# Performance work log

Measured on AMD Instinct MI355X. Metric: run time of the kernel, lower is better.

The kernel has to match this reference:

```python
import jax, jax.numpy as jnp
import numpy as np

B, T, D, H = 2, 2048, 2048, 16
HS = D // H  # head size 128


def setup_inputs() -> dict:
    key = jax.random.key(0)
    ks = jax.random.split(key, 5)
    s = 0.02
    return {
        "x": jax.random.normal(ks[0], (B, T, D), dtype=jnp.float32),
        "wq": jax.random.normal(ks[1], (D, D), dtype=jnp.float32) * s,
        "wk": jax.random.normal(ks[2], (D, D), dtype=jnp.float32) * s,
        "wv": jax.random.normal(ks[3], (D, D), dtype=jnp.float32) * s,
        "wo": jax.random.normal(ks[4], (D, D), dtype=jnp.float32) * s,
    }


def reference(x, wq, wk, wv, wo):
    b, t, d = x.shape
    # projections: nn.Linear(x) = x @ W.T ; here W stored as (out,in)
    q = (x @ wq.T).reshape(b, t, H, HS).transpose(0, 2, 1, 3)  # (B,H,T,HS)
    k = (x @ wk.T).reshape(b, t, H, HS).transpose(0, 2, 1, 3)
    v = (x @ wv.T).reshape(b, t, H, HS).transpose(0, 2, 1, 3)
    scale = 1.0 / np.sqrt(HS).astype(np.float32)
    e = jnp.einsum("bhqd,bhkd->bhqk", q, k) * scale  # (B,H,T,T)
    causal = jnp.tril(jnp.ones((t, t), dtype=bool))
    e = jnp.where(causal[None, None], e, jnp.float32(-jnp.inf))
    alpha = jax.nn.softmax(e, axis=-1)  # dropout=0.0 -> identity
    attn = jnp.einsum("bhqk,bhkd->bhqd", alpha, v)
    attn = attn.transpose(0, 2, 1, 3).reshape(b, t, d)
    return attn @ wo.T
```

## Files before the change

kernel.cpp:

```cpp
#include <hip/hip_runtime.h>
#include <hip/hip_bf16.h>

typedef __bf16 bf16x8 __attribute__((ext_vector_type(8)));
typedef float f32x4 __attribute__((ext_vector_type(4)));
typedef unsigned short u16x8 __attribute__((ext_vector_type(8)));

#define GLDS16(g, s)                                                         \
  __builtin_amdgcn_global_load_lds(                                          \
      (const __attribute__((address_space(1))) void*)(g),                    \
      (__attribute__((address_space(3))) void*)(s), 16, 0, 0)

__device__ __forceinline__ void store1(__hip_bfloat16* p, float v) { *p = __float2bfloat16(v); }
__device__ __forceinline__ void store1(float* p, float v) { *p = v; }

__global__ __launch_bounds__(256) void cast_f32_to_bf16(const float4* __restrict__ in,
                                                        ushort4* __restrict__ out, int n4) {
  int i = blockIdx.x * 256 + threadIdx.x;
  if (i >= n4) return;
  float4 v = in[i];
  union { ushort4 u; __hip_bfloat16 h[4]; } o;
  o.h[0] = __float2bfloat16(v.x);
  o.h[1] = __float2bfloat16(v.y);
  o.h[2] = __float2bfloat16(v.z);
  o.h[3] = __float2bfloat16(v.w);
  out[i] = o.u;
}

__global__ __launch_bounds__(256) void cast4_f32_to_bf16(const float4* __restrict__ w0,
                                                         const float4* __restrict__ w1,
                                                         const float4* __restrict__ w2,
                                                         const float4* __restrict__ w3,
                                                         ushort4* __restrict__ o0,
                                                         ushort4* __restrict__ o1,
                                                         ushort4* __restrict__ o2,
                                                         ushort4* __restrict__ o3, int n4) {
  int i = blockIdx.x * 256 + threadIdx.x;
  if (i >= n4) return;
  int s = blockIdx.y;
  const float4* in = (s == 0) ? w0 : (s == 1) ? w1 : (s == 2) ? w2 : w3;
  ushort4* out = (s == 0) ? o0 : (s == 1) ? o1 : (s == 2) ? o2 : o3;
  float4 v = in[i];
  union { ushort4 u; __hip_bfloat16 h[4]; } o;
  o.h[0] = __float2bfloat16(v.x);
  o.h[1] = __float2bfloat16(v.y);
  o.h[2] = __float2bfloat16(v.z);
  o.h[3] = __float2bfloat16(v.w);
  out[i] = o.u;
}

template <typename OutT>
__global__ __launch_bounds__(512, 2) void gemm256(const __hip_bfloat16* __restrict__ A,
                                                  const __hip_bfloat16* __restrict__ B0,
                                                  const __hip_bfloat16* __restrict__ B1,
                                                  const __hip_bfloat16* __restrict__ B2,
                                                  OutT* __restrict__ C0,
                                                  OutT* __restrict__ C1,
                                                  OutT* __restrict__ C2,
                                                  int nBx, int nBy, int ntPerMat,
                                                  int N, int K) {
  __shared__ __hip_bfloat16 As[2][256 * 64];
  __shared__ __hip_bfloat16 Bs[2][256 * 64];

  const int t = threadIdx.x;
  const int w = t >> 6, l = t & 63;
  const int lr = l & 15, hi = l >> 4;

  const int nwg = nBx * nBy;
  int id = (int)blockIdx.x;
  id = (id & 7) * (nwg >> 3) + (id >> 3);
  const int bx = id / nBy;
  const int by = id % nBy;

  const int sel = bx / ntPerMat;
  const __hip_bfloat16* Bm = (sel == 0) ? B0 : ((sel == 1) ? B1 : B2);
  OutT* Cm = (sel == 0) ? C0 : ((sel == 1) ? C1 : C2);
  const int n0 = (bx - sel * ntPerMat) * 256;
  const int m0 = by * 256;

  const int c0r = t >> 3, cs = t & 7;
  const int c1r = 64 + c0r;
  const __hip_bfloat16* aP0 = A + (size_t)(m0 + c0r) * K + (cs ^ (c0r & 7)) * 8;
  const __hip_bfloat16* aP1 = A + (size_t)(m0 + c1r) * K + (cs ^ (c1r & 7)) * 8;
  const __hip_bfloat16* bP0 = Bm + (size_t)(n0 + c0r) * K + (cs ^ (c0r & 7)) * 8;
  const __hip_bfloat16* bP1 = Bm + (size_t)(n0 + c1r) * K + (cs ^ (c1r & 7)) * 8;
  const size_t HK = (size_t)128 * K;

#define STAGE_S(sidx, nb, koff)                                              \
  do {                                                                       \
    if ((sidx) == 0) {                                                       \
      GLDS16(aP0 + (koff), (char*)As[nb] + t * 16);                          \
      GLDS16(aP1 + (koff), (char*)As[nb] + 8192 + t * 16);                   \
    } else if ((sidx) == 1) {                                                \
      GLDS16(bP0 + (koff), (char*)Bs[nb] + t * 16);                          \
      GLDS16(bP1 + (koff), (char*)Bs[nb] + 8192 + t * 16);                   \
    } else if ((sidx) == 2) {                                                \
      GLDS16(aP0 + HK + (koff), (char*)As[nb] + 16384 + t * 16);             \
      GLDS16(aP1 + HK + (koff), (char*)As[nb] + 24576 + t * 16);             \
    } else {                                                                 \
      GLDS16(bP0 + HK + (koff), (char*)Bs[nb] + 16384 + t * 16);             \
      GLDS16(bP1 + HK + (koff), (char*)Bs[nb] + 24576 + t * 16);             \
    }                                                                        \
  } while (0)

  f32x4 acc[2][2][4][2] = {};
  bf16x8 afA[4][2], afB[4][2];
  bf16x8 bqA[2][2], bqB[2][2];
  const int NT = K / 64;
  const int sw = lr & 7;
  const int arow = (w >> 2) * 64;
  const int brow = (w & 3) * 32;

#define RD_A(dst, mh)                                                        \
  _Pragma("unroll") for (int mi = 0; mi < 4; ++mi)                           \
    _Pragma("unroll") for (int kk = 0; kk < 2; ++kk)                         \
      dst[mi][kk] = *(const bf16x8*)((const char*)As[buf] +                  \
          ((mh) * 128 + arow + mi * 16 + lr) * 128 + (((kk * 4 + hi) ^ sw) << 4));
#define RD_B(dst, nh)                                                        \
  _Pragma("unroll") for (int ni = 0; ni < 2; ++ni)                           \
    _Pragma("unroll") for (int kk = 0; kk < 2; ++kk)                         \
      dst[ni][kk] = *(const bf16x8*)((const char*)Bs[buf] +                  \
          ((nh) * 128 + brow + ni * 16 + lr) * 128 + (((kk * 4 + hi) ^ sw) << 4));
#define MFMA_Q(mh, nh, afv, bq)                                              \
  do {                                                                       \
    __builtin_amdgcn_s_setprio(1);                                           \
    _Pragma("unroll") for (int mi = 0; mi < 4; ++mi)                         \
      _Pragma("unroll") for (int ni = 0; ni < 2; ++ni) {                     \
        acc[mh][nh][mi][ni] = __builtin_amdgcn_mfma_f32_16x16x32_bf16(       \
            afv[mi][0], bq[ni][0], acc[mh][nh][mi][ni], 0, 0, 0);            \
        acc[mh][nh][mi][ni] = __builtin_amdgcn_mfma_f32_16x16x32_bf16(       \
            afv[mi][1], bq[ni][1], acc[mh][nh][mi][ni], 0, 0, 0);            \
      }                                                                      \
    __builtin_amdgcn_s_setprio(0);                                           \
  } while (0)
#define WAITV(n)  asm volatile("s_waitcnt vmcnt(" #n ")" ::: "memory")

  STAGE_S(0, 0, 0);
  STAGE_S(1, 0, 0);
  STAGE_S(3, 0, 0);
  STAGE_S(2, 0, 0);

  for (int tt = 0; tt < NT; ++tt) {
    const int buf = tt & 1, nb = buf ^ 1;
    const bool stg = (tt + 1 < NT);
    const size_t ko = (size_t)(tt + 1) * 64;

    WAITV(2);
    __builtin_amdgcn_s_barrier();
    RD_A(afA, 0);
    RD_B(bqA, 0);
    RD_B(bqB, 1);
    if (stg) { STAGE_S(0, nb, ko); STAGE_S(1, nb, ko); }
    MFMA_Q(0, 0, afA, bqA);
    MFMA_Q(0, 1, afA, bqB);

    if (stg) WAITV(4); else WAITV(0);
    __builtin_amdgcn_s_barrier();
    RD_A(afB, 1);
    if (stg) { STAGE_S(3, nb, ko); STAGE_S(2, nb, ko); }
    MFMA_Q(1, 1, afB, bqB);
    MFMA_Q(1, 0, afB, bqA);
  }
#undef WAITV
#undef MFMA_Q
#undef RD_B
#undef RD_A
#undef STAGE_S

#pragma unroll
  for (int mh = 0; mh < 2; ++mh)
#pragma unroll
    for (int nh = 0; nh < 2; ++nh)
#pragma unroll
      for (int mi = 0; mi < 4; ++mi)
#pragma unroll
        for (int ni = 0; ni < 2; ++ni)
#pragma unroll
          for (int i = 0; i < 4; ++i) {
            size_t idx = (size_t)(m0 + mh * 128 + arow + mi * 16 + hi * 4 + i) * N +
                         (n0 + nh * 128 + brow + ni * 16 + lr);
            store1(&Cm[idx], acc[mh][nh][mi][ni][i]);
          }
}

__global__ __launch_bounds__(256, 2) void flash_attn(const __hip_bfloat16* __restrict__ Qg,
                                                     const __hip_bfloat16* __restrict__ Kg,
                                                     const __hip_bfloat16* __restrict__ Vg,
                                                     __hip_bfloat16* __restrict__ Og) {
  __shared__ __hip_bfloat16 Ks[2][64 * 128];
  __shared__ __hip_bfloat16 Vt[128 * 64];

  const int mblk = blockIdx.x;
  const int bh = mblk & 31;
  const int jj = mblk >> 5;
  const int qt = (jj < 8) ? (15 - jj) : (jj - 8);
  const int b = bh >> 4, h = bh & 15;
  const int q0 = qt * 128;
  const int t = threadIdx.x, w = t >> 6, l = t & 63;
  const int lr = l & 15, hi = l >> 4;
  const size_t base = ((size_t)b * 2048) * 2048 + (size_t)h * 128;
  const int nt = 2 * qt + 2;
  const float scale = 0.08838834764831843f;

  const int hi2 = (hi & 1) * 2;
  const int addrA = (((hi2) << 4) | lr) << 2;
  const int addrB = (((hi2 + 1) << 4) | lr) << 2;
  int addr_o[4];
#pragma unroll
  for (int i = 0; i < 4; ++i) addr_o[i] = ((l & 48) | (hi * 4 + i)) << 2;
  const bool hiHigh = (hi >> 1) != 0;

  bf16x8 qf[2][4];
#pragma unroll
  for (int g = 0; g < 2; ++g) {
    const __hip_bfloat16* qrow = Qg + base + (size_t)(q0 + w * 32 + g * 16 + lr) * 2048;
#pragma unroll
    for (int kk = 0; kk < 4; ++kk)
      qf[g][kk] = *(const bf16x8*)(qrow + kk * 32 + hi * 8);
  }

  f32x4 o_acc[2][8] = {};
  float m_run[2] = {-1e30f, -1e30f};
  float l_run[2] = {0.f, 0.f};

  const __hip_bfloat16* kptr[4];
#pragma unroll
  for (int i = 0; i < 4; ++i) {
    int c = i * 256 + t;
    int kr = c >> 4;
    int ke = ((c & 15) ^ (kr & 7)) * 8;
    kptr[i] = Kg + base + (size_t)kr * 2048 + ke;
  }
  const __hip_bfloat16* vptr[2];
#pragma unroll
  for (int it = 0; it < 2; ++it) {
    int kp = it * 16 + w * 4 + hi;
    vptr[it] = Vg + base + (size_t)(kp * 2) * 2048 + lr * 8;
  }

  u16x8 va[2], vb[2];
#pragma unroll
  for (int i = 0; i < 4; ++i)
    GLDS16(kptr[i], (char*)Ks[0] + (i * 256 + t) * 16);
#pragma unroll
  for (int it = 0; it < 2; ++it) {
    va[it] = *(const u16x8*)vptr[it];
    vb[it] = *(const u16x8*)(vptr[it] + 2048);
  }

  for (int kt = 0; kt < nt; ++kt) {
    const int cur = kt & 1;
    const int kb = kt * 64;
    __syncthreads();

#pragma unroll
    for (int it = 0; it < 2; ++it)
#pragma unroll
      for (int j2 = 0; j2 < 8; ++j2) {
        int d = lr * 8 + j2;
        int sw = (lr ^ j2) & 7;
        int off = d * 128 + (((it * 4 + w) ^ sw) << 4) + hi * 4;
        *(unsigned int*)((char*)Vt + off) =
            (unsigned int)va[it][j2] | ((unsigned int)vb[it][j2] << 16);
      }
    if (kt + 1 < nt) {
      const size_t adv = (size_t)(kb + 64) * 2048;
#pragma unroll
      for (int i = 0; i < 4; ++i)
        GLDS16(kptr[i] + adv, (char*)Ks[cur ^ 1] + (i * 256 + t) * 16);
#pragma unroll
      for (int it = 0; it < 2; ++it) {
        va[it] = *(const u16x8*)(vptr[it] + adv);
        vb[it] = *(const u16x8*)(vptr[it] + adv + 2048);
      }
    }
    asm volatile("s_waitcnt lgkmcnt(0)" ::: "memory");
    __builtin_amdgcn_s_barrier();

    if (!(kt == nt - 1 && w < 2)) {
      const char* ks = (const char*)Ks[cur];

      f32x4 st[2][4];
#pragma unroll
      for (int g = 0; g < 2; ++g)
#pragma unroll
        for (int nk = 0; nk < 4; ++nk) { f32x4 z = {}; st[g][nk] = z; }
#pragma unroll
      for (int nk = 0; nk < 4; ++nk)
#pragma unroll
        for (int kk = 0; kk < 4; ++kk) {
          bf16x8 kf = *(const bf16x8*)(ks + (nk * 16 + lr) * 256 +
                                       (((kk * 4 + hi) ^ (lr & 7)) << 4));
#pragma unroll
          for (int g = 0; g < 2; ++g)
            st[g][nk] = __builtin_amdgcn_mfma_f32_16x16x32_bf16(kf, qf[g][kk], st[g][nk], 0, 0, 0);
        }

      const bool maskt = (kt >= nt - 2);
#pragma unroll
      for (int g = 0; g < 2; ++g)
#pragma unroll
        for (int nk = 0; nk < 4; ++nk)
#pragma unroll
          for (int i = 0; i < 4; ++i) {
            float v = st[g][nk][i] * scale;
            if (maskt) {
              int ki = kb + nk * 16 + hi * 4 + i;
              int qi = q0 + w * 32 + g * 16 + lr;
              if (ki > qi) v = -1e30f;
            }
            st[g][nk][i] = v;
          }

      bf16x8 paf[2][2];
#pragma unroll
      for (int g = 0; g < 2; ++g) {
        float t0 = fmaxf(fmaxf(st[g][0][0], st[g][0][1]), fmaxf(st[g][0][2], st[g][0][3]));
        float t1 = fmaxf(fmaxf(st[g][1][0], st[g][1][1]), fmaxf(st[g][1][2], st[g][1][3]));
        float t2 = fmaxf(fmaxf(st[g][2][0], st[g][2][1]), fmaxf(st[g][2][2], st[g][2][3]));
        float t3 = fmaxf(fmaxf(st[g][3][0], st[g][3][1]), fmaxf(st[g][3][2], st[g][3][3]));
        float mx = fmaxf(fmaxf(t0, t1), fmaxf(t2, t3));
        mx = fmaxf(mx, __shfl_xor(mx, 16));
        mx = fmaxf(mx, __shfl_xor(mx, 32));

        if (!__all(mx - m_run[g] <= 8.0f)) {
          float mnew = fmaxf(m_run[g], mx);
          float rs = __expf(m_run[g] - mnew);
          m_run[g] = mnew;
          l_run[g] *= rs;
          int rsi = __float_as_int(rs);
#pragma unroll
          for (int i = 0; i < 4; ++i) {
            float rso = __int_as_float(__builtin_amdgcn_ds_bpermute(addr_o[i], rsi));
#pragma unroll
            for (int nc = 0; nc < 8; ++nc) o_acc[g][nc][i] *= rso;
          }
        }

#pragma unroll
        for (int nk = 0; nk < 4; ++nk)
#pragma unroll
          for (int i = 0; i < 4; ++i)
            st[g][nk][i] = __expf(st[g][nk][i] - m_run[g]);

        float s0 = (st[g][0][0] + st[g][0][1]) + (st[g][0][2] + st[g][0][3]);
        float s1 = (st[g][1][0] + st[g][1][1]) + (st[g][1][2] + st[g][1][3]);
        float s2 = (st[g][2][0] + st[g][2][1]) + (st[g][2][2] + st[g][2][3]);
        float s3 = (st[g][3][0] + st[g][3][1]) + (st[g][3][2] + st[g][3][3]);
        float sm = (s0 + s1) + (s2 + s3);
        sm += __shfl_xor(sm, 16);
        sm += __shfl_xor(sm, 32);
        l_run[g] += sm;

        unsigned pk[4][2];
#pragma unroll
        for (int nk = 0; nk < 4; ++nk) {
          asm("v_cvt_pk_bf16_f32 %0, %1, %2"
              : "=v"(pk[nk][0]) : "v"(st[g][nk][0]), "v"(st[g][nk][1]));
          asm("v_cvt_pk_bf16_f32 %0, %1, %2"
              : "=v"(pk[nk][1]) : "v"(st[g][nk][2]), "v"(st[g][nk][3]));
        }

#pragma unroll
        for (int kk = 0; kk < 2; ++kk) {
          unsigned au[4];
#pragma unroll
          for (int p = 0; p < 4; ++p) {
            int ad = (p < 2) ? addrA : addrB;
            int v0 = __builtin_amdgcn_ds_bpermute(ad, (int)pk[2 * kk][p & 1]);
            int v1 = __builtin_amdgcn_ds_bpermute(ad, (int)pk[2 * kk + 1][p & 1]);
            au[p] = hiHigh ? (unsigned)v1 : (unsigned)v0;
          }
          union { unsigned u[4]; bf16x8 v; } cv;
          cv.u[0] = au[0]; cv.u[1] = au[1]; cv.u[2] = au[2]; cv.u[3] = au[3];
          paf[g][kk] = cv.v;
        }
      }

#pragma unroll
      for (int kk = 0; kk < 2; ++kk)
#pragma unroll
        for (int nc = 0; nc < 8; ++nc) {
          int d = nc * 16 + lr;
          int sw = ((d >> 3) ^ d) & 7;
          bf16x8 vfr = *(const bf16x8*)((const char*)Vt + d * 128 +
                                        (((kk * 4 + hi) ^ sw) << 4));
#pragma unroll
          for (int g = 0; g < 2; ++g)
            o_acc[g][nc] = __builtin_amdgcn_mfma_f32_16x16x32_bf16(paf[g][kk], vfr, o_acc[g][nc], 0, 0, 0);
        }
    }
  }

#pragma unroll
  for (int g = 0; g < 2; ++g) {
    float lo[4];
#pragma unroll
    for (int i = 0; i < 4; ++i)
      lo[i] = __int_as_float(__builtin_amdgcn_ds_bpermute(addr_o[i], __float_as_int(l_run[g])));
#pragma unroll
    for (int nc = 0; nc < 8; ++nc)
#pragma unroll
      for (int i = 0; i < 4; ++i) {
        float val = o_acc[g][nc][i] / lo[i];
        Og[base + (size_t)(q0 + w * 32 + g * 16 + hi * 4 + i) * 2048 + nc * 16 + lr] =
            __float2bfloat16(val);
      }
  }
}

extern "C" void kernel_launch(void* const* d_in, const int* in_sizes, int n_in,
                              void* d_out, int out_size, void* d_ws, size_t ws_size,
                              hipStream_t stream) {
  const float* x  = (const float*)d_in[0];
  const float* wq = (const float*)d_in[1];
  const float* wk = (const float*)d_in[2];
  const float* wv = (const float*)d_in[3];
  const float* wo = (const float*)d_in[4];
  float* out = (float*)d_out;

  const int BT = 4096, D = 2048;
  const size_t ND = (size_t)D * D;
  const size_t NX = (size_t)BT * D;

  __hip_bfloat16* xb  = (__hip_bfloat16*)d_ws;
  __hip_bfloat16* wqb = xb + NX;
  __hip_bfloat16* wkb = wqb + ND;
  __hip_bfloat16* wvb = wkb + ND;
  __hip_bfloat16* wob = wvb + ND;
  __hip_bfloat16* Qb  = wob + ND;
  __hip_bfloat16* Kb  = Qb + NX;
  __hip_bfloat16* Vb  = Kb + NX;
  __hip_bfloat16* Ab  = Vb + NX;

  cast_f32_to_bf16<<<(int)(NX / 4 / 256), 256, 0, stream>>>((const float4*)x, (ushort4*)xb, (int)(NX / 4));
  cast4_f32_to_bf16<<<dim3((int)(ND / 4 / 256), 4), 256, 0, stream>>>(
      (const float4*)wq, (const float4*)wk, (const float4*)wv, (const float4*)wo,
      (ushort4*)wqb, (ushort4*)wkb, (ushort4*)wvb, (ushort4*)wob, (int)(ND / 4));

  gemm256<__hip_bfloat16><<<384, 512, 0, stream>>>(
      xb, wqb, wkb, wvb, Qb, Kb, Vb, 24, 16, 8, D, D);

  flash_attn<<<512, 256, 0, stream>>>(Qb, Kb, Vb, Ab);

  gemm256<float><<<128, 512, 0, stream>>>(
      Ab, wob, wob, wob, out, out, out, 8, 16, 8, D, D);
}
```

Before: 282.1 us.

## Issue all next-tile loads upfront and prefetch LDS fragments into registers

After: 282.8 us. No clear change (+0.2%).

```diff
diff --git a/kernel.cpp b/kernel.cpp
--- a/kernel.cpp
+++ b/kernel.cpp
@@ -110,15 +110,15 @@
   const int arow = (w >> 2) * 64;
   const int brow = (w & 3) * 32;
 
-#define RD_A(dst, mh)                                                        \
+#define RD_A(dst, mh, bb)                                                    \
   _Pragma("unroll") for (int mi = 0; mi < 4; ++mi)                           \
     _Pragma("unroll") for (int kk = 0; kk < 2; ++kk)                         \
-      dst[mi][kk] = *(const bf16x8*)((const char*)As[buf] +                  \
+      dst[mi][kk] = *(const bf16x8*)((const char*)As[bb] +                   \
           ((mh) * 128 + arow + mi * 16 + lr) * 128 + (((kk * 4 + hi) ^ sw) << 4));
-#define RD_B(dst, nh)                                                        \
+#define RD_B(dst, nh, bb)                                                    \
   _Pragma("unroll") for (int ni = 0; ni < 2; ++ni)                           \
     _Pragma("unroll") for (int kk = 0; kk < 2; ++kk)                         \
-      dst[ni][kk] = *(const bf16x8*)((const char*)Bs[buf] +                  \
+      dst[ni][kk] = *(const bf16x8*)((const char*)Bs[bb] +                   \
           ((nh) * 128 + brow + ni * 16 + lr) * 128 + (((kk * 4 + hi) ^ sw) << 4));
 #define MFMA_Q(mh, nh, afv, bq)                                              \
   do {                                                                       \
@@ -138,27 +138,40 @@
   STAGE_S(1, 0, 0);
   STAGE_S(3, 0, 0);
   STAGE_S(2, 0, 0);
+  WAITV(0);
+  __builtin_amdgcn_s_barrier();
+  RD_A(afA, 0, 0);
+  RD_B(bqA, 0, 0);
+  RD_B(bqB, 1, 0);
 
   for (int tt = 0; tt < NT; ++tt) {
     const int buf = tt & 1, nb = buf ^ 1;
     const bool stg = (tt + 1 < NT);
     const size_t ko = (size_t)(tt + 1) * 64;
 
-    WAITV(2);
+    if (stg) {
+      STAGE_S(0, nb, ko);
+      STAGE_S(1, nb, ko);
+      STAGE_S(3, nb, ko);
+      STAGE_S(2, nb, ko);
+      WAITV(8);
+    } else {
+      WAITV(0);
+    }
     __builtin_amdgcn_s_barrier();
-    RD_A(afA, 0);
-    RD_B(bqA, 0);
-    RD_B(bqB, 1);
-    if (stg) { STAGE_S(0, nb, ko); STAGE_S(1, nb, ko); }
     MFMA_Q(0, 0, afA, bqA);
     MFMA_Q(0, 1, afA, bqB);
-
-    if (stg) WAITV(4); else WAITV(0);
+    RD_A(afB, 1, buf);
+
+    if (stg) WAITV(2); else WAITV(0);
     __builtin_amdgcn_s_barrier();
-    RD_A(afB, 1);
-    if (stg) { STAGE_S(3, nb, ko); STAGE_S(2, nb, ko); }
     MFMA_Q(1, 1, afB, bqB);
     MFMA_Q(1, 0, afB, bqA);
+    if (stg) {
+      RD_A(afA, 0, nb);
+      RD_B(bqA, 0, nb);
+      RD_B(bqB, 1, nb);
+    }
   }
 #undef WAITV
 #undef MFMA_Q
```

## Triple-buffer K and double-buffer V in flash attention to deepen prefetch

Applied to the files above, without the earlier changes.

Result: slower. 296.4 us (+5.1%).

```diff
diff --git a/kernel.cpp b/kernel.cpp
--- a/kernel.cpp
+++ b/kernel.cpp
@@ -186,8 +186,8 @@
                                                      const __hip_bfloat16* __restrict__ Kg,
                                                      const __hip_bfloat16* __restrict__ Vg,
                                                      __hip_bfloat16* __restrict__ Og) {
-  __shared__ __hip_bfloat16 Ks[2][64 * 128];
-  __shared__ __hip_bfloat16 Vt[128 * 64];
+  __shared__ __hip_bfloat16 Ks[3][64 * 128];
+  __shared__ __hip_bfloat16 Vt[2][128 * 64];
 
   const int mblk = blockIdx.x;
   const int bh = mblk & 31;
@@ -237,49 +237,55 @@
     vptr[it] = Vg + base + (size_t)(kp * 2) * 2048 + lr * 8;
   }
 
-  u16x8 va[2], vb[2];
+#define WRITE_VT(vbuf, a, bmat)                                              \
+  _Pragma("unroll") for (int it = 0; it < 2; ++it)                           \
+    _Pragma("unroll") for (int j2 = 0; j2 < 8; ++j2) {                       \
+      int d = lr * 8 + j2;                                                   \
+      int swz = (lr ^ j2) & 7;                                               \
+      int off = d * 128 + (((it * 4 + w) ^ swz) << 4) + hi * 4;              \
+      *(unsigned int*)((char*)Vt[vbuf] + off) =                              \
+          (unsigned)a[it][j2] | ((unsigned)bmat[it][j2] << 16);              \
+    }
+
 #pragma unroll
   for (int i = 0; i < 4; ++i)
     GLDS16(kptr[i], (char*)Ks[0] + (i * 256 + t) * 16);
-#pragma unroll
-  for (int it = 0; it < 2; ++it) {
-    va[it] = *(const u16x8*)vptr[it];
-    vb[it] = *(const u16x8*)(vptr[it] + 2048);
+  {
+    u16x8 wa[2], wb[2];
+#pragma unroll
+    for (int it = 0; it < 2; ++it) {
+      wa[it] = *(const u16x8*)vptr[it];
+      wb[it] = *(const u16x8*)(vptr[it] + 2048);
+    }
+    WRITE_VT(0, wa, wb);
+  }
+  u16x8 va[2], vbr[2];
+  {
+    const size_t adv = (size_t)64 * 2048;
+#pragma unroll
+    for (int i = 0; i < 4; ++i)
+      GLDS16(kptr[i] + adv, (char*)Ks[1] + (i * 256 + t) * 16);
+#pragma unroll
+    for (int it = 0; it < 2; ++it) {
+      va[it] = *(const u16x8*)(vptr[it] + adv);
+      vbr[it] = *(const u16x8*)(vptr[it] + adv + 2048);
+    }
   }
 
   for (int kt = 0; kt < nt; ++kt) {
-    const int cur = kt & 1;
+    const int kcur = kt % 3;
+    const int vcur = kt & 1;
     const int kb = kt * 64;
-    __syncthreads();
-
-#pragma unroll
-    for (int it = 0; it < 2; ++it)
-#pragma unroll
-      for (int j2 = 0; j2 < 8; ++j2) {
-        int d = lr * 8 + j2;
-        int sw = (lr ^ j2) & 7;
-        int off = d * 128 + (((it * 4 + w) ^ sw) << 4) + hi * 4;
-        *(unsigned int*)((char*)Vt + off) =
-            (unsigned int)va[it][j2] | ((unsigned int)vb[it][j2] << 16);
-      }
-    if (kt + 1 < nt) {
-      const size_t adv = (size_t)(kb + 64) * 2048;
-#pragma unroll
-      for (int i = 0; i < 4; ++i)
-        GLDS16(kptr[i] + adv, (char*)Ks[cur ^ 1] + (i * 256 + t) * 16);
-#pragma unroll
-      for (int it = 0; it < 2; ++it) {
-        va[it] = *(const u16x8*)(vptr[it] + adv);
-        vb[it] = *(const u16x8*)(vptr[it] + adv + 2048);
-      }
-    }
-    asm volatile("s_waitcnt lgkmcnt(0)" ::: "memory");
+
+    if (kt + 1 < nt) asm volatile("s_waitcnt vmcnt(8)" ::: "memory");
+    else             asm volatile("s_waitcnt vmcnt(0)" ::: "memory");
     __builtin_amdgcn_s_barrier();
 
-    if (!(kt == nt - 1 && w < 2)) {
-      const char* ks = (const char*)Ks[cur];
-
-      f32x4 st[2][4];
+    const bool active = !(kt == nt - 1 && w < 2);
+    const char* ks = (const char*)Ks[kcur];
+
+    f32x4 st[2][4];
+    if (active) {
 #pragma unroll
       for (int g = 0; g < 2; ++g)
 #pragma unroll
@@ -294,7 +300,23 @@
           for (int g = 0; g < 2; ++g)
             st[g][nk] = __builtin_amdgcn_mfma_f32_16x16x32_bf16(kf, qf[g][kk], st[g][nk], 0, 0, 0);
         }
-
+    }
+
+    if (kt + 1 < nt) { WRITE_VT(vcur ^ 1, va, vbr); }
+
+    if (kt + 2 < nt) {
+      const size_t adv = (size_t)(kb + 128) * 2048;
+#pragma unroll
+      for (int i = 0; i < 4; ++i)
+        GLDS16(kptr[i] + adv, (char*)Ks[(kt + 2) % 3] + (i * 256 + t) * 16);
+#pragma unroll
+      for (int it = 0; it < 2; ++it) {
+        va[it] = *(const u16x8*)(vptr[it] + adv);
+        vbr[it] = *(const u16x8*)(vptr[it] + adv + 2048);
+      }
+    }
+
+    if (active) {
       const bool maskt = (kt >= nt - 2);
 #pragma unroll
       for (int g = 0; g < 2; ++g)
@@ -381,14 +403,16 @@
 #pragma unroll
         for (int nc = 0; nc < 8; ++nc) {
           int d = nc * 16 + lr;
-          int sw = ((d >> 3) ^ d) & 7;
-          bf16x8 vfr = *(const bf16x8*)((const char*)Vt + d * 128 +
-                                        (((kk * 4 + hi) ^ sw) << 4));
+          int swz = ((d >> 3) ^ d) & 7;
+          bf16x8 vfr = *(const bf16x8*)((const char*)Vt[vcur] + d * 128 +
+                                        (((kk * 4 + hi) ^ swz) << 4));
 #pragma unroll
           for (int g = 0; g < 2; ++g)
             o_acc[g][nc] = __builtin_amdgcn_mfma_f32_16x16x32_bf16(paf[g][kk], vfr, o_acc[g][nc], 0, 0, 0);
         }
     }
+
+    asm volatile("s_waitcnt lgkmcnt(0)" ::: "memory");
   }
 
 #pragma unroll
@@ -406,6 +430,7 @@
             __float2bfloat16(val);
       }
   }
+#undef WRITE_VT
 }
 
 extern "C" void kernel_launch(void* const* d_in, const int* in_sizes, int n_in,
```

## Shrink GEMM tile to 128x256 with triple-buffered LDS pipeline

Applied to the files above, without the earlier changes.

Result: no change. 277.6 us (-1.6%).

```diff
diff --git a/kernel.cpp b/kernel.cpp
--- a/kernel.cpp
+++ b/kernel.cpp
@@ -58,8 +58,8 @@
                                                   OutT* __restrict__ C2,
                                                   int nBx, int nBy, int ntPerMat,
                                                   int N, int K) {
-  __shared__ __hip_bfloat16 As[2][256 * 64];
-  __shared__ __hip_bfloat16 Bs[2][256 * 64];
+  __shared__ __hip_bfloat16 As[3][128 * 64];
+  __shared__ __hip_bfloat16 Bs[3][256 * 64];
 
   const int t = threadIdx.x;
   const int w = t >> 6, l = t & 63;
@@ -75,7 +75,7 @@
   const __hip_bfloat16* Bm = (sel == 0) ? B0 : ((sel == 1) ? B1 : B2);
   OutT* Cm = (sel == 0) ? C0 : ((sel == 1) ? C1 : C2);
   const int n0 = (bx - sel * ntPerMat) * 256;
-  const int m0 = by * 256;
+  const int m0 = by * 128;
 
   const int c0r = t >> 3, cs = t & 7;
   const int c1r = 64 + c0r;
@@ -85,101 +85,83 @@
   const __hip_bfloat16* bP1 = Bm + (size_t)(n0 + c1r) * K + (cs ^ (c1r & 7)) * 8;
   const size_t HK = (size_t)128 * K;
 
-#define STAGE_S(sidx, nb, koff)                                              \
+#define STAGE_T(bb, koff)                                                    \
   do {                                                                       \
-    if ((sidx) == 0) {                                                       \
-      GLDS16(aP0 + (koff), (char*)As[nb] + t * 16);                          \
-      GLDS16(aP1 + (koff), (char*)As[nb] + 8192 + t * 16);                   \
-    } else if ((sidx) == 1) {                                                \
-      GLDS16(bP0 + (koff), (char*)Bs[nb] + t * 16);                          \
-      GLDS16(bP1 + (koff), (char*)Bs[nb] + 8192 + t * 16);                   \
-    } else if ((sidx) == 2) {                                                \
-      GLDS16(aP0 + HK + (koff), (char*)As[nb] + 16384 + t * 16);             \
-      GLDS16(aP1 + HK + (koff), (char*)As[nb] + 24576 + t * 16);             \
-    } else {                                                                 \
-      GLDS16(bP0 + HK + (koff), (char*)Bs[nb] + 16384 + t * 16);             \
-      GLDS16(bP1 + HK + (koff), (char*)Bs[nb] + 24576 + t * 16);             \
-    }                                                                        \
+    GLDS16(aP0 + (koff), (char*)As[bb] + t * 16);                            \
+    GLDS16(aP1 + (koff), (char*)As[bb] + 8192 + t * 16);                     \
+    GLDS16(bP0 + (koff), (char*)Bs[bb] + t * 16);                            \
+    GLDS16(bP1 + (koff), (char*)Bs[bb] + 8192 + t * 16);                     \
+    GLDS16(bP0 + HK + (koff), (char*)Bs[bb] + 16384 + t * 16);               \
+    GLDS16(bP1 + HK + (koff), (char*)Bs[bb] + 24576 + t * 16);               \
   } while (0)
 
-  f32x4 acc[2][2][4][2] = {};
-  bf16x8 afA[4][2], afB[4][2];
+  f32x4 acc[2][4][2] = {};
+  bf16x8 afA[4][2];
   bf16x8 bqA[2][2], bqB[2][2];
   const int NT = K / 64;
   const int sw = lr & 7;
   const int arow = (w >> 2) * 64;
   const int brow = (w & 3) * 32;
 
-#define RD_A(dst, mh)                                                        \
+#define RD_A(dst)                                                            \
   _Pragma("unroll") for (int mi = 0; mi < 4; ++mi)                           \
     _Pragma("unroll") for (int kk = 0; kk < 2; ++kk)                         \
       dst[mi][kk] = *(const bf16x8*)((const char*)As[buf] +                  \
-          ((mh) * 128 + arow + mi * 16 + lr) * 128 + (((kk * 4 + hi) ^ sw) << 4));
+          (arow + mi * 16 + lr) * 128 + (((kk * 4 + hi) ^ sw) << 4));
 #define RD_B(dst, nh)                                                        \
   _Pragma("unroll") for (int ni = 0; ni < 2; ++ni)                           \
     _Pragma("unroll") for (int kk = 0; kk < 2; ++kk)                         \
       dst[ni][kk] = *(const bf16x8*)((const char*)Bs[buf] +                  \
           ((nh) * 128 + brow + ni * 16 + lr) * 128 + (((kk * 4 + hi) ^ sw) << 4));
-#define MFMA_Q(mh, nh, afv, bq)                                              \
+#define MFMA_Q(nh, afv, bq)                                                  \
   do {                                                                       \
     __builtin_amdgcn_s_setprio(1);                                           \
     _Pragma("unroll") for (int mi = 0; mi < 4; ++mi)                         \
       _Pragma("unroll") for (int ni = 0; ni < 2; ++ni) {                     \
-        acc[mh][nh][mi][ni] = __builtin_amdgcn_mfma_f32_16x16x32_bf16(       \
-            afv[mi][0], bq[ni][0], acc[mh][nh][mi][ni], 0, 0, 0);            \
-        acc[mh][nh][mi][ni] = __builtin_amdgcn_mfma_f32_16x16x32_bf16(       \
-            afv[mi][1], bq[ni][1], acc[mh][nh][mi][ni], 0, 0, 0);            \
+        acc[nh][mi][ni] = __builtin_amdgcn_mfma_f32_16x16x32_bf16(           \
+            afv[mi][0], bq[ni][0], acc[nh][mi][ni], 0, 0, 0);                \
+        acc[nh][mi][ni] = __builtin_amdgcn_mfma_f32_16x16x32_bf16(           \
+            afv[mi][1], bq[ni][1], acc[nh][mi][ni], 0, 0, 0);                \
       }                                                                      \
     __builtin_amdgcn_s_setprio(0);                                           \
   } while (0)
 #define WAITV(n)  asm volatile("s_waitcnt vmcnt(" #n ")" ::: "memory")
 
-  STAGE_S(0, 0, 0);
-  STAGE_S(1, 0, 0);
-  STAGE_S(3, 0, 0);
-  STAGE_S(2, 0, 0);
+  STAGE_T(0, 0);
+  STAGE_T(1, 64);
 
   for (int tt = 0; tt < NT; ++tt) {
-    const int buf = tt & 1, nb = buf ^ 1;
-    const bool stg = (tt + 1 < NT);
-    const size_t ko = (size_t)(tt + 1) * 64;
-
-    WAITV(2);
+    const int buf = tt % 3;
+
+    if (tt + 1 < NT) WAITV(6); else WAITV(0);
     __builtin_amdgcn_s_barrier();
-    RD_A(afA, 0);
+
+    RD_A(afA);
     RD_B(bqA, 0);
     RD_B(bqB, 1);
-    if (stg) { STAGE_S(0, nb, ko); STAGE_S(1, nb, ko); }
-    MFMA_Q(0, 0, afA, bqA);
-    MFMA_Q(0, 1, afA, bqB);
-
-    if (stg) WAITV(4); else WAITV(0);
-    __builtin_amdgcn_s_barrier();
-    RD_A(afB, 1);
-    if (stg) { STAGE_S(3, nb, ko); STAGE_S(2, nb, ko); }
-    MFMA_Q(1, 1, afB, bqB);
-    MFMA_Q(1, 0, afB, bqA);
+    if (tt + 2 < NT) STAGE_T((tt + 2) % 3, (size_t)(tt + 2) * 64);
+
+    MFMA_Q(0, afA, bqA);
+    MFMA_Q(1, afA, bqB);
   }
 #undef WAITV
 #undef MFMA_Q
 #undef RD_B
 #undef RD_A
-#undef STAGE_S
-
-#pragma unroll
-  for (int mh = 0; mh < 2; ++mh)
-#pragma unroll
-    for (int nh = 0; nh < 2; ++nh)
-#pragma unroll
-      for (int mi = 0; mi < 4; ++mi)
-#pragma unroll
-        for (int ni = 0; ni < 2; ++ni)
-#pragma unroll
-          for (int i = 0; i < 4; ++i) {
-            size_t idx = (size_t)(m0 + mh * 128 + arow + mi * 16 + hi * 4 + i) * N +
-                         (n0 + nh * 128 + brow + ni * 16 + lr);
-            store1(&Cm[idx], acc[mh][nh][mi][ni][i]);
-          }
+#undef STAGE_T
+
+#pragma unroll
+  for (int nh = 0; nh < 2; ++nh)
+#pragma unroll
+    for (int mi = 0; mi < 4; ++mi)
+#pragma unroll
+      for (int ni = 0; ni < 2; ++ni)
+#pragma unroll
+        for (int i = 0; i < 4; ++i) {
+          size_t idx = (size_t)(m0 + arow + mi * 16 + hi * 4 + i) * N +
+                       (n0 + nh * 128 + brow + ni * 16 + lr);
+          store1(&Cm[idx], acc[nh][mi][ni][i]);
+        }
 }
 
 __global__ __launch_bounds__(256, 2) void flash_attn(const __hip_bfloat16* __restrict__ Qg,
@@ -437,11 +419,11 @@
       (const float4*)wq, (const float4*)wk, (const float4*)wv, (const float4*)wo,
       (ushort4*)wqb, (ushort4*)wkb, (ushort4*)wvb, (ushort4*)wob, (int)(ND / 4));
 
-  gemm256<__hip_bfloat16><<<384, 512, 0, stream>>>(
-      xb, wqb, wkb, wvb, Qb, Kb, Vb, 24, 16, 8, D, D);
+  gemm256<__hip_bfloat16><<<768, 512, 0, stream>>>(
+      xb, wqb, wkb, wvb, Qb, Kb, Vb, 24, 32, 8, D, D);
 
   flash_attn<<<512, 256, 0, stream>>>(Qb, Kb, Vb, Ab);
 
-  gemm256<float><<<128, 512, 0, stream>>>(
-      Ab, wob, wob, wob, out, out, out, 8, 16, 8, D, D);
+  gemm256<float><<<256, 512, 0, stream>>>(
+      Ab, wob, wob, wob, out, out, out, 8, 32, 8, D, D);
 }
```
